# Performance work log

Measured on AMD Instinct MI355X. Metric: run time of the kernel, lower is better.

The kernel has to match this reference:

```python
import jax, jax.numpy as jnp
import numpy as np

B, IN_C, OUT_C, K, Z_DIM = 32, 128, 128, 3, 512
H, W, STRIDE = 56, 56, 1


def setup_inputs() -> dict:
    key = jax.random.key(0)
    k1, k2, k3 = jax.random.split(key, 3)
    x = jax.random.normal(k1, (B, IN_C, H, W), dtype=jnp.float32)
    z = jax.random.normal(k2, (B, Z_DIM), dtype=jnp.float32)
    # nn.Linear(z_dim, out_c*in_c*k*k): weight [out_f, in_f], bias [out_f]
    out_f = OUT_C * IN_C * K * K
    W_head = jax.random.normal(k3, (out_f, Z_DIM), dtype=jnp.float32) * (1.0 / np.sqrt(Z_DIM))
    b_head = jnp.zeros((out_f,), dtype=jnp.float32)
    return {"x": x, "z": z, "W_head": W_head, "b_head": b_head}


def reference(x, z, W_head, b_head):
    b = x.shape[0]
    # hypernetwork head: per-sample conv weights
    w = z @ W_head.T + b_head                       # [B, out_c*in_c*k*k]
    w = w.reshape(b, OUT_C, IN_C, K, K)             # [B, O, I, K, K]

    pad = K // 2

    def conv_one(xi, wi):
        # xi: [I, H, W], wi: [O, I, K, K] -> [O, H', W']
        out = jax.lax.conv_general_dilated(
            xi[None],                                # [1, I, H, W]
            wi,
            window_strides=(STRIDE, STRIDE),
            padding=[(pad, pad), (pad, pad)],
            dimension_numbers=("NCHW", "OIHW", "NCHW"),
        )
        return out[0]

    return jax.vmap(conv_one)(x, w)                 # [B, O, H', W']
```

## Files before the change

kernel.cpp:

```cpp
#include <hip/hip_runtime.h>
#include <hip/hip_bf16.h>
#include <stdint.h>

#define BB 32
#define IC 128
#define OC 128
#define HH 56
#define WW 56
#define ZD 512
#define NRS 9
#define OI (OC*IC)
#define WROWS (OI*NRS)
#define WDIM 58

typedef float  f32x4  __attribute__((ext_vector_type(4)));
typedef short  bf16x8 __attribute__((ext_vector_type(8)));

static __device__ __forceinline__ short f2bf(float f) {
    uint32_t u = __float_as_uint(f);
    uint32_t r = (u + 0x7fffu + ((u >> 16) & 1u)) >> 16;
    return (short)r;
}
static __device__ __forceinline__ short f2bf_hw(float f) {
    __hip_bfloat16 h = __float2bfloat16(f);
    return *reinterpret_cast<short*>(&h);
}
static __device__ __forceinline__ float bf2f(short s) {
    uint32_t u = ((uint32_t)(uint16_t)s) << 16;
    return __uint_as_float(u);
}
static __device__ __forceinline__ void gll16(const void* g, void* l) {
    __builtin_amdgcn_global_load_lds(
        (const __attribute__((address_space(1))) uint32_t*)g,
        (__attribute__((address_space(3))) uint32_t*)l, 16, 0, 0);
}

__global__ __launch_bounds__(256) void head_kernel(
    const float* __restrict__ Wh, const float* __restrict__ z,
    short* __restrict__ wnat)
{
    __shared__ __align__(16) char Zl[32 * 1024];
    __shared__ __align__(16) char Wl[4][2][4096];
    const int tid  = threadIdx.x;
    const int lane = tid & 63;
    const int wv   = tid >> 6;

    {
        const int b = tid >> 3, ks = (tid & 7) * 64;
        const float* zp = z + (size_t)b * ZD + ks;
        const int bx = (b & 7) << 4;
        #pragma unroll
        for (int j8 = 0; j8 < 8; ++j8) {
            f32x4 v0 = *(const f32x4*)(zp + j8 * 8);
            f32x4 v1 = *(const f32x4*)(zp + j8 * 8 + 4);
            bf16x8 pk;
            pk[0] = f2bf_hw(v0.x); pk[1] = f2bf_hw(v0.y);
            pk[2] = f2bf_hw(v0.z); pk[3] = f2bf_hw(v0.w);
            pk[4] = f2bf_hw(v1.x); pk[5] = f2bf_hw(v1.y);
            pk[6] = f2bf_hw(v1.z); pk[7] = f2bf_hw(v1.w);
            *(bf16x8*)(Zl + b * 1024 + ((ks * 2 + j8 * 16) ^ bx)) = pk;
        }
    }
    __syncthreads();

    const int rl = lane & 15;
    const int kq = lane >> 4;
    const int zxor = (rl & 7) << 4;
    const int row0 = blockIdx.x * 64 + wv * 16;

    const float* lsrc = Wh + (size_t)(row0 + kq) * ZD + (lane & 15) * 4;
    char* WT = (char*)Wl[wv][0];

    #define LOADC(c, R)                                                         \
        _Pragma("unroll")                                                       \
        for (int j = 0; j < 4; ++j)                                             \
            R[j] = *(const f32x4*)(lsrc + (size_t)(j * 4) * ZD + (c) * 64);

    #define WRC(buf, R)                                                         \
        _Pragma("unroll")                                                       \
        for (int j = 0; j < 4; ++j) {                                           \
            const int row_ = j * 4 + kq;                                        \
            *(f32x4*)(WT + (buf) * 4096 + row_ * 256 +                          \
                      (((lane & 15) * 16) ^ ((row_ & 7) << 4))) = R[j];         \
        }

    f32x4 RA[4], RB[4];
    LOADC(0, RA);
    LOADC(1, RB);
    WRC(0, RA);

    f32x4 acc0 = {0.f, 0.f, 0.f, 0.f}, acc1 = {0.f, 0.f, 0.f, 0.f};

    #pragma unroll
    for (int c = 0; c < 8; ++c) {
        if (c + 2 < 8) {
            if ((c & 1) == 0) { LOADC(c + 2, RA); }
            else              { LOADC(c + 2, RB); }
        }
        #pragma unroll
        for (int ks = 0; ks < 2; ++ks) {
            const int koff = (c * 128 + ks * 64 + kq * 16) ^ zxor;
            bf16x8 a0 = *(const bf16x8*)(Zl + rl * 1024 + koff);
            bf16x8 a1 = *(const bf16x8*)(Zl + (16 + rl) * 1024 + koff);
            const char* wb = WT + (c & 1) * 4096 + rl * 256;
            f32x4 lo = *(const f32x4*)(wb + ((ks * 128 + kq * 32) ^ zxor));
            f32x4 hi = *(const f32x4*)(wb + ((ks * 128 + kq * 32 + 16) ^ zxor));
            bf16x8 bw;
            bw[0] = f2bf_hw(lo.x); bw[1] = f2bf_hw(lo.y);
            bw[2] = f2bf_hw(lo.z); bw[3] = f2bf_hw(lo.w);
            bw[4] = f2bf_hw(hi.x); bw[5] = f2bf_hw(hi.y);
            bw[6] = f2bf_hw(hi.z); bw[7] = f2bf_hw(hi.w);
            acc0 = __builtin_amdgcn_mfma_f32_16x16x32_bf16(a0, bw, acc0, 0, 0, 0);
            acc1 = __builtin_amdgcn_mfma_f32_16x16x32_bf16(a1, bw, acc1, 0, 0, 0);
        }
        if (c + 1 < 8) {
            if ((c & 1) == 0) { WRC(1, RB); }
            else              { WRC(0, RA); }
        }
    }
    #undef LOADC
    #undef WRC

    const int rowg = row0 + rl;
    #pragma unroll
    for (int reg = 0; reg < 4; ++reg) {
        const int b0 = kq * 4 + reg;
        wnat[(size_t)b0 * WROWS + rowg]        = f2bf(acc0[reg]);
        wnat[(size_t)(16 + b0) * WROWS + rowg] = f2bf(acc1[reg]);
    }
}

__global__ __launch_bounds__(256) void repack_kernel(
    const short* __restrict__ wnat, const float* __restrict__ bh,
    short* __restrict__ wbf)
{
    const int b = blockIdx.y;
    const int oi0 = blockIdx.x * 2048 + threadIdx.x * 8;
    const short* src = wnat + (size_t)b * WROWS + (size_t)oi0 * 9;
    const float* bp  = bh + (size_t)oi0 * 9;

    bf16x8 in[9];
    #pragma unroll
    for (int j = 0; j < 9; ++j) in[j] = *(const bf16x8*)(src + j * 8);
    f32x4 bv[18];
    #pragma unroll
    for (int m = 0; m < 18; ++m) bv[m] = *(const f32x4*)(bp + m * 4);

    #pragma unroll
    for (int rs = 0; rs < 9; ++rs) {
        bf16x8 o;
        #pragma unroll
        for (int jj = 0; jj < 8; ++jj) {
            const int e = jj * 9 + rs;
            float v = bf2f(in[e >> 3][e & 7]) + bv[e >> 2][e & 3];
            o[jj] = f2bf(v);
        }
        *(bf16x8*)(wbf + ((size_t)(b * 9 + rs)) * OI + oi0) = o;
    }
}

__global__ __launch_bounds__(256) void transpose_kernel(
    const float* __restrict__ x, short* __restrict__ xt)
{
    const int h = blockIdx.x;
    const int b = blockIdx.y;
    const int w = threadIdx.x & 63;
    const int yq = threadIdx.x >> 6;
    if (w >= WW) return;
    const float* xp = x + (size_t)b * IC * HH * WW + h * WW + w;
    short* op = xt + (((size_t)(b * HH + h)) * WW + w) * IC;
    #pragma unroll
    for (int q = 0; q < 4; ++q) {
        int ic = yq * 4 + q;
        bf16x8 pk;
        #pragma unroll
        for (int j = 0; j < 8; ++j) {
            float v = xp[(size_t)(ic * 8 + j) * (HH * WW)];
            pk[j] = f2bf(v);
        }
        *(bf16x8*)(op + ic * 8) = pk;
    }
}

__global__ __launch_bounds__(256) void conv_kernel(
    const short* __restrict__ wbf,
    const short* __restrict__ xt,
    float* __restrict__ out)
{
    __shared__ __align__(16) char Xl[3 * WDIM * 256];
    __shared__ __align__(16) char Wl[128 * 256];
    const int tid  = threadIdx.x;
    const int lane = tid & 63;
    const int wv   = tid >> 6;
    const int h = blockIdx.x;
    const int b = blockIdx.y;

    #pragma unroll
    for (int q = 0; q < 11; ++q) {
        int idx = tid + q * 256;
        if (idx < 3 * WDIM * 16) ((f32x4*)Xl)[idx] = (f32x4){0.f, 0.f, 0.f, 0.f};
    }
    __syncthreads();

    for (int r = 0; r < 3; ++r) {
        int hin = h + r - 1;
        if (hin < 0 || hin >= HH) continue;
        const char* src = (const char*)(xt + ((size_t)(b * HH + hin)) * WW * IC);
        char* dstbase = Xl + (r * WDIM + 1) * 256;
        for (int it = wv; it < 14; it += 4) {
            int c = it * 64 + lane;
            int u = r * WDIM + 1 + (c >> 4);
            int soff = (c * 16) ^ ((u & 7) << 4);
            gll16(src + soff, dstbase + it * 1024);
        }
    }

    f32x4 acc[2][4];
    #pragma unroll
    for (int a = 0; a < 2; ++a)
        #pragma unroll
        for (int p = 0; p < 4; ++p) acc[a][p] = (f32x4){0.f, 0.f, 0.f, 0.f};

    const int axor = (lane & 7) << 4;
    int kkoff[4];
    #pragma unroll
    for (int kk = 0; kk < 4; ++kk) kkoff[kk] = kk * 64 + ((lane >> 4) << 4);

    for (int rs = 0; rs < 9; ++rs) {
        __syncthreads();
        const char* wsrc = (const char*)(wbf + ((size_t)b * NRS + rs) * OI);
        for (int it = wv; it < 32; it += 4) {
            int c = it * 64 + lane;
            int soff = (c * 16) ^ (((c >> 4) & 7) << 4);
            gll16(wsrc + soff, Wl + it * 1024);
        }
        __syncthreads();

        const int r = rs / 3, s = rs - 3 * (rs / 3);
        int ubase[4], bswz[4];
        #pragma unroll
        for (int pf = 0; pf < 4; ++pf) {
            int p = pf * 16 + (lane & 15);
            int pc = p > 55 ? 55 : p;
            int uu = r * WDIM + pc + s;
            ubase[pf] = uu * 256;
            bswz[pf] = (uu & 7) << 4;
        }
        #pragma unroll
        for (int kk = 0; kk < 4; ++kk) {
            bf16x8 a0 = *(const bf16x8*)(Wl + (wv * 32 + (lane & 15)) * 256 +
                                         (kkoff[kk] ^ axor));
            bf16x8 a1 = *(const bf16x8*)(Wl + (wv * 32 + 16 + (lane & 15)) * 256 +
                                         (kkoff[kk] ^ axor));
            #pragma unroll
            for (int pf = 0; pf < 4; ++pf) {
                bf16x8 bv = *(const bf16x8*)(Xl + ubase[pf] + (kkoff[kk] ^ bswz[pf]));
                acc[0][pf] = __builtin_amdgcn_mfma_f32_16x16x32_bf16(a0, bv, acc[0][pf], 0, 0, 0);
                acc[1][pf] = __builtin_amdgcn_mfma_f32_16x16x32_bf16(a1, bv, acc[1][pf], 0, 0, 0);
            }
        }
    }

    const int pcol = lane & 15;
    const int rowq = lane >> 4;
    #pragma unroll
    for (int a = 0; a < 2; ++a) {
        int o0 = wv * 32 + a * 16 + rowq * 4;
        #pragma unroll
        for (int pf = 0; pf < 4; ++pf) {
            int p = pf * 16 + pcol;
            if (p < WW) {
                #pragma unroll
                for (int reg = 0; reg < 4; ++reg) {
                    out[(((size_t)b * OC + (o0 + reg)) * HH + h) * WW + p] = acc[a][pf][reg];
                }
            }
        }
    }
}

extern "C" void kernel_launch(void* const* d_in, const int* in_sizes, int n_in,
                              void* d_out, int out_size, void* d_ws, size_t ws_size,
                              hipStream_t stream) {
    const float* x  = (const float*)d_in[0];
    const float* z  = (const float*)d_in[1];
    const float* Wh = (const float*)d_in[2];
    const float* bh = (const float*)d_in[3];
    float* out = (float*)d_out;

    short* wnat = (short*)d_ws;
    short* wbf  = (short*)((char*)d_ws + 9437184);
    short* xt   = (short*)((char*)d_ws + 18874368);

    head_kernel<<<dim3(WROWS / 64), 256, 0, stream>>>(Wh, z, wnat);
    repack_kernel<<<dim3(8, 32), 256, 0, stream>>>(wnat, bh, wbf);
    transpose_kernel<<<dim3(HH, BB), 256, 0, stream>>>(x, xt);
    conv_kernel<<<dim3(HH, BB), 256, 0, stream>>>(wbf, xt, out);
}
```

Before: 168.9 us.

## Fuse transpose into hypernetwork head launch and load head weights directly to registers

Merges the input transpose blocks into the head GEMM kernel as extra grid blocks, which removes one launch and lets the two independent jobs overlap on the device. The head GEMM drops its LDS double-buffered staging of W_head and instead has each lane load its whole 512-float row slice straight into 32 vector registers before running the MFMA loop. The costs are higher register pressure (launch bounds now ask for 2 blocks) and less coalesced global loads. A stray label statement is left in the launch function.

```diff
diff --git a/kernel.cpp b/kernel.cpp
--- a/kernel.cpp
+++ b/kernel.cpp
@@ -12,6 +12,8 @@
 #define OI (OC*IC)
 #define WROWS (OI*NRS)
 #define WDIM 58
+#define NHEADBLK (WROWS / 64)
+#define NTRBLK (HH * BB)
 
 typedef float  f32x4  __attribute__((ext_vector_type(4)));
 typedef short  bf16x8 __attribute__((ext_vector_type(8)));
@@ -35,12 +37,35 @@
         (__attribute__((address_space(3))) uint32_t*)l, 16, 0, 0);
 }
 
-__global__ __launch_bounds__(256) void head_kernel(
+__global__ __launch_bounds__(256, 2) void fused_head_tr_kernel(
     const float* __restrict__ Wh, const float* __restrict__ z,
-    short* __restrict__ wnat)
+    short* __restrict__ wnat,
+    const float* __restrict__ x, short* __restrict__ xt)
 {
+    if (blockIdx.x >= NHEADBLK) {
+        const int bx = blockIdx.x - NHEADBLK;
+        const int b = bx / HH;
+        const int h = bx - b * HH;
+        const int w = threadIdx.x & 63;
+        const int yq = threadIdx.x >> 6;
+        if (w >= WW) return;
+        const float* xp = x + (size_t)b * IC * HH * WW + h * WW + w;
+        short* op = xt + (((size_t)(b * HH + h)) * WW + w) * IC;
+        #pragma unroll
+        for (int q = 0; q < 4; ++q) {
+            int ic = yq * 4 + q;
+            bf16x8 pk;
+            #pragma unroll
+            for (int j = 0; j < 8; ++j) {
+                float v = xp[(size_t)(ic * 8 + j) * (HH * WW)];
+                pk[j] = f2bf(v);
+            }
+            *(bf16x8*)(op + ic * 8) = pk;
+        }
+        return;
+    }
+
     __shared__ __align__(16) char Zl[32 * 1024];
-    __shared__ __align__(16) char Wl[4][2][4096];
     const int tid  = threadIdx.x;
     const int lane = tid & 63;
     const int wv   = tid >> 6;
@@ -66,62 +91,34 @@
     const int rl = lane & 15;
     const int kq = lane >> 4;
     const int zxor = (rl & 7) << 4;
-    const int row0 = blockIdx.x * 64 + wv * 16;
-
-    const float* lsrc = Wh + (size_t)(row0 + kq) * ZD + (lane & 15) * 4;
-    char* WT = (char*)Wl[wv][0];
-
-    #define LOADC(c, R)                                                         \
-        _Pragma("unroll")                                                       \
-        for (int j = 0; j < 4; ++j)                                             \
-            R[j] = *(const f32x4*)(lsrc + (size_t)(j * 4) * ZD + (c) * 64);
-
-    #define WRC(buf, R)                                                         \
-        _Pragma("unroll")                                                       \
-        for (int j = 0; j < 4; ++j) {                                           \
-            const int row_ = j * 4 + kq;                                        \
-            *(f32x4*)(WT + (buf) * 4096 + row_ * 256 +                          \
-                      (((lane & 15) * 16) ^ ((row_ & 7) << 4))) = R[j];         \
-        }
-
-    f32x4 RA[4], RB[4];
-    LOADC(0, RA);
-    LOADC(1, RB);
-    WRC(0, RA);
+    const int rowg = blockIdx.x * 64 + wv * 16 + rl;
+
+    const char* wp = (const char*)Wh + (size_t)rowg * (ZD * 4) + kq * 32;
+
+    f32x4 wd[32];
+    #pragma unroll
+    for (int i = 0; i < 16; ++i) {
+        wd[2 * i]     = *(const f32x4*)(wp + i * 128);
+        wd[2 * i + 1] = *(const f32x4*)(wp + i * 128 + 16);
+    }
 
     f32x4 acc0 = {0.f, 0.f, 0.f, 0.f}, acc1 = {0.f, 0.f, 0.f, 0.f};
-
-    #pragma unroll
-    for (int c = 0; c < 8; ++c) {
-        if (c + 2 < 8) {
-            if ((c & 1) == 0) { LOADC(c + 2, RA); }
-            else              { LOADC(c + 2, RB); }
-        }
-        #pragma unroll
-        for (int ks = 0; ks < 2; ++ks) {
-            const int koff = (c * 128 + ks * 64 + kq * 16) ^ zxor;
-            bf16x8 a0 = *(const bf16x8*)(Zl + rl * 1024 + koff);
-            bf16x8 a1 = *(const bf16x8*)(Zl + (16 + rl) * 1024 + koff);
-            const char* wb = WT + (c & 1) * 4096 + rl * 256;
-            f32x4 lo = *(const f32x4*)(wb + ((ks * 128 + kq * 32) ^ zxor));
-            f32x4 hi = *(const f32x4*)(wb + ((ks * 128 + kq * 32 + 16) ^ zxor));
-            bf16x8 bw;
-            bw[0] = f2bf_hw(lo.x); bw[1] = f2bf_hw(lo.y);
-            bw[2] = f2bf_hw(lo.z); bw[3] = f2bf_hw(lo.w);
-            bw[4] = f2bf_hw(hi.x); bw[5] = f2bf_hw(hi.y);
-            bw[6] = f2bf_hw(hi.z); bw[7] = f2bf_hw(hi.w);
-            acc0 = __builtin_amdgcn_mfma_f32_16x16x32_bf16(a0, bw, acc0, 0, 0, 0);
-            acc1 = __builtin_amdgcn_mfma_f32_16x16x32_bf16(a1, bw, acc1, 0, 0, 0);
-        }
-        if (c + 1 < 8) {
-            if ((c & 1) == 0) { WRC(1, RB); }
-            else              { WRC(0, RA); }
-        }
-    }
-    #undef LOADC
-    #undef WRC
-
-    const int rowg = row0 + rl;
+    #pragma unroll
+    for (int kb = 0; kb < 16; ++kb) {
+        const int koff = (kb * 64 + kq * 16) ^ zxor;
+        bf16x8 a0 = *(const bf16x8*)(Zl + rl * 1024 + koff);
+        bf16x8 a1 = *(const bf16x8*)(Zl + (16 + rl) * 1024 + koff);
+        f32x4 lo = wd[2 * kb];
+        f32x4 hi = wd[2 * kb + 1];
+        bf16x8 bw;
+        bw[0] = f2bf_hw(lo.x); bw[1] = f2bf_hw(lo.y);
+        bw[2] = f2bf_hw(lo.z); bw[3] = f2bf_hw(lo.w);
+        bw[4] = f2bf_hw(hi.x); bw[5] = f2bf_hw(hi.y);
+        bw[6] = f2bf_hw(hi.z); bw[7] = f2bf_hw(hi.w);
+        acc0 = __builtin_amdgcn_mfma_f32_16x16x32_bf16(a0, bw, acc0, 0, 0, 0);
+        acc1 = __builtin_amdgcn_mfma_f32_16x16x32_bf16(a1, bw, acc1, 0, 0, 0);
+    }
+
     #pragma unroll
     for (int reg = 0; reg < 4; ++reg) {
         const int b0 = kq * 4 + reg;
@@ -156,29 +153,6 @@
             o[jj] = f2bf(v);
         }
         *(bf16x8*)(wbf + ((size_t)(b * 9 + rs)) * OI + oi0) = o;
-    }
-}
-
-__global__ __launch_bounds__(256) void transpose_kernel(
-    const float* __restrict__ x, short* __restrict__ xt)
-{
-    const int h = blockIdx.x;
-    const int b = blockIdx.y;
-    const int w = threadIdx.x & 63;
-    const int yq = threadIdx.x >> 6;
-    if (w >= WW) return;
-    const float* xp = x + (size_t)b * IC * HH * WW + h * WW + w;
-    short* op = xt + (((size_t)(b * HH + h)) * WW + w) * IC;
-    #pragma unroll
-    for (int q = 0; q < 4; ++q) {
-        int ic = yq * 4 + q;
-        bf16x8 pk;
-        #pragma unroll
-        for (int j = 0; j < 8; ++j) {
-            float v = xp[(size_t)(ic * 8 + j) * (HH * WW)];
-            pk[j] = f2bf(v);
-        }
-        *(bf16x8*)(op + ic * 8) = pk;
     }
 }
 
@@ -292,8 +266,8 @@
     short* wbf  = (short*)((char*)d_ws + 9437184);
     short* xt   = (short*)((char*)d_ws + 18874368);
 
-    head_kernel<<<dim3(WROWS / 64), 256, 0, stream>>>(Wh, z, wnat);
+    fused_head_tr_kernel<<<dim3(NHEADBLK + NTRBLK), 256, 0, stream>>>(Wh, z, wnat, x, xt);
     repack_kernel<<<dim3(8, 32), 256, 0, stream>>>(wnat, bh, wbf);
-    transpose_kernel<<<dim3(HH, BB), 256, 0, stream>>>(x, xt);
+    transpose_kernel_dummy:;
     conv_kernel<<<dim3(HH, BB), 256, 0, stream>>>(wbf, xt, out);
 }
```

After: 164.1 us. 2.8% less time.
